# Optimization experiments

Measured on AMD Instinct MI355X. Metric: run time of the kernel, lower is better.

The kernel has to match this reference:

```python
import jax, jax.numpy as jnp
import numpy as np
from jax import lax

KSIZE = 7

def _grid():
    # torch.linspace(-7//2, 7//2, 7) == linspace(-4, 3, 7): asymmetric, step 7/6
    x = np.linspace(-4.0, 3.0, KSIZE, dtype=np.float32).reshape(-1, 1)
    y = x.T
    return x, y

def _gaussian_kernel(sigma):
    x, y = _grid()
    g = np.exp(-(x ** 2 + y ** 2) / (2.0 * sigma ** 2))
    g = g / g.sum()
    return g.reshape(1, 1, KSIZE, KSIZE).astype(np.float32)

def _log_kernel(sigma):
    x, y = _grid()
    r2 = x ** 2 + y ** 2
    log = (1.0 - r2 / (2.0 * sigma ** 2)) * np.exp(-r2 / (2.0 * sigma ** 2))
    log = log / np.abs(log).sum()
    return log.reshape(1, 1, KSIZE, KSIZE).astype(np.float32)

SOBEL_X = jnp.asarray([[-1, 0, 1], [-2, 0, 2], [-1, 0, 1]], dtype=jnp.float32).reshape(1, 1, 3, 3)
SOBEL_Y = jnp.asarray([[-1, -2, -1], [0, 0, 0], [1, 2, 1]], dtype=jnp.float32).reshape(1, 1, 3, 3)
POINT = jnp.asarray([[0, -1, 0], [-1, 4, -1], [0, -1, 0]], dtype=jnp.float32).reshape(1, 1, 3, 3)
STRUCT_FILTERS = [jnp.asarray(_gaussian_kernel(s)) for s in (0.5, 1.0, 2.0)]
SCALE_FILTERS = [jnp.asarray(_log_kernel(s)) for s in (1.0, 2.0, 4.0)]

def _conv(x, k, pad):
    # torch F.conv2d == cross-correlation, which lax conv also computes (no kernel flip)
    return lax.conv_general_dilated(
        x, k, window_strides=(1, 1),
        padding=[(pad, pad), (pad, pad)],
        dimension_numbers=("NCHW", "OIHW", "NCHW"))

def _mse(a, b):
    d = a - b
    return jnp.mean(d * d)

def _maxpool3(x):
    # torch max_pool2d pads with -inf
    return lax.reduce_window(
        x, -jnp.inf, lax.max,
        window_dimensions=(1, 1, 3, 3), window_strides=(1, 1, 1, 1),
        padding=[(0, 0), (0, 0), (1, 1), (1, 1)])

def setup_inputs() -> dict:
    key = jax.random.key(0)
    k1, k2 = jax.random.split(key)
    shape = (64, 1, 512, 512)
    return {
        "reconstruction": jax.random.normal(k1, shape, dtype=jnp.float32),
        "target": jax.random.normal(k2, shape, dtype=jnp.float32),
    }

def reference(reconstruction, target):
    # intensity-weighted reconstruction loss
    w = (target > target.mean()).astype(reconstruction.dtype) * 2.0 + 1.0
    recon_loss = _mse(reconstruction * w, target * w)

    # gradient (sobel) loss
    gradient_loss = (
        _mse(_conv(reconstruction, SOBEL_X, 1), _conv(target, SOBEL_X, 1)) +
        _mse(_conv(reconstruction, SOBEL_Y, 1), _conv(target, SOBEL_Y, 1)))

    # point-source (laplacian) loss
    point_loss = _mse(_conv(reconstruction, POINT, 1), _conv(target, POINT, 1))

    # multi-scale gaussian structure loss
    structure_loss = 0.0
    for f in STRUCT_FILTERS:
        structure_loss += _mse(_conv(reconstruction, f, KSIZE // 2), _conv(target, f, KSIZE // 2))

    # LoG blob-scale loss
    scale_loss = 0.0
    for f in SCALE_FILTERS:
        scale_loss += _mse(_conv(reconstruction, f, KSIZE // 2), _conv(target, f, KSIZE // 2))

    # peak preservation via 3x3 max pool + L1
    peak_loss = jnp.mean(jnp.abs(_maxpool3(reconstruction) - _maxpool3(target)))

    return (recon_loss + 2.0 * gradient_loss + 1.5 * point_loss +
            1.0 * structure_loss + 1.0 * scale_loss + 2.0 * peak_loss)
```

## Files before the change

### kernel.cpp

```cpp
#include <hip/hip_runtime.h>
#include <math.h>

#define IMG 512
#define IMG2 (IMG * IMG)
#define NPIX (64 * IMG2)
#define ZPB 8

__device__ float g_c[64];

typedef __fp16 h2_t __attribute__((ext_vector_type(2)));

#define OOB_SRT 0xFBFFFBFFu

__device__ __forceinline__ float rdfl(float x) {
    return __uint_as_float(__builtin_amdgcn_readfirstlane(__float_as_uint(x)));
}
__device__ __forceinline__ unsigned int rdflu(float x) {
    return __builtin_amdgcn_readfirstlane(__float_as_uint(x));
}
__device__ __forceinline__ unsigned int as_u(h2_t h) {
    union { h2_t h; unsigned int u; } c;
    c.h = h;
    return c.u;
}
__device__ __forceinline__ h2_t as_h2(unsigned int u) {
    union { unsigned int u; h2_t h; } c;
    c.u = u;
    return c.h;
}
__device__ __forceinline__ h2_t h2z() {
    h2_t z = {(__fp16)0.f, (__fp16)0.f};
    return z;
}
__device__ __forceinline__ h2_t hmax2(h2_t a, h2_t b) {
    return __builtin_elementwise_max(a, b);
}

__device__ void compute_coeffs() {
    const double step = 7.0 / 6.0;
    float x[7];
    for (int j = 0; j < 7; j++) x[j] = (float)(-4.0 + j * step);
    x[6] = 3.0f;
    const float sigs[4] = {0.5f, 1.0f, 2.0f, 4.0f};
    float E[4][7], Q[4][7], Vv[3][7];
    for (int s = 0; s < 4; s++) {
        float inv = 1.0f / (2.0f * sigs[s] * sigs[s]);
        for (int j = 0; j < 7; j++) {
            float q = x[j] * x[j] * inv;
            Q[s][j] = q;
            E[s][j] = expf(-q);
        }
    }
    for (int s = 0; s < 3; s++)
        for (int j = 0; j < 7; j++) Vv[s][j] = Q[s + 1][j] * E[s + 1][j];

    auto pk2 = [](float a, float b) -> float {
        h2_t h;
        h[0] = (__fp16)a;
        h[1] = (__fp16)b;
        union { h2_t h; float f; } c;
        c.h = h;
        return c.f;
    };
    for (int k = 0; k < 7; k++) {
        g_c[k] = pk2(E[0][k], E[1][k]);
        g_c[7 + k] = pk2(E[2][k], E[3][k]);
        g_c[14 + k] = pk2(Vv[0][k], Vv[1][k]);
        g_c[21 + k] = pk2(Vv[2][k], Vv[2][k]);
        g_c[28 + k] = pk2(E[1][k], E[2][k]);
        g_c[35 + k] = pk2(E[2][k], -Vv[2][k]);
        g_c[42 + k] = pk2(-Vv[0][k], -Vv[1][k]);
        g_c[49 + k] = pk2(E[3][k], 0.f);
    }
    for (int s = 0; s < 3; s++) {
        float gs = 0.f;
        for (int i = 0; i < 7; i++)
            for (int j = 0; j < 7; j++) gs += E[s][i] * E[s][j];
        g_c[56 + s] = 1.0f / (gs * gs);
    }
    for (int s = 1; s < 4; s++) {
        float n = 0.f;
        for (int i = 0; i < 7; i++)
            for (int j = 0; j < 7; j++) {
                float v = E[s][i] * E[s][j] * (1.0f - Q[s][i] - Q[s][j]);
                n += fabsf(v);
            }
        g_c[59 + (s - 1)] = 1.0f / (n * n);
    }
}

__global__ __launch_bounds__(256) void sum_target_kernel(const float4* __restrict__ t4,
                                                          float* __restrict__ ws) {
    if (blockIdx.x == 0 && threadIdx.x == 0) compute_coeffs();
    float s = 0.f;
    for (int i = blockIdx.x * 256 + threadIdx.x; i < NPIX / 4; i += 256 * 256) {
        float4 v = t4[i];
        s += (v.x + v.y) + (v.z + v.w);
    }
    for (int off = 32; off > 0; off >>= 1) s += __shfl_down(s, off);
    __shared__ float ps[4];
    int lane = threadIdx.x & 63, wid = threadIdx.x >> 6;
    if (lane == 0) ps[wid] = s;
    __syncthreads();
    if (threadIdx.x == 0) ws[blockIdx.x] = (ps[0] + ps[1]) + (ps[2] + ps[3]);
}

__global__ __launch_bounds__(256, 6) void main_kernel(const float* __restrict__ R,
                                                      const float* __restrict__ T,
                                                      float* __restrict__ ws) {
    __shared__ unsigned srt[38][44];
    __shared__ uint4 hrec[32][39];
    __shared__ float red[4];

    const int tid = threadIdx.x;
    const int gx0 = blockIdx.x * 32, gy0 = blockIdx.y * 32;
    const int z0 = blockIdx.z * ZPB;
    const int bid = blockIdx.x + (blockIdx.y << 4) + (blockIdx.z << 8);

    {
        float v = ws[tid];
        for (int off = 32; off > 0; off >>= 1) v += __shfl_down(v, off);
        int lane = tid & 63, wid = tid >> 6;
        if (lane == 0) red[wid] = v;
        __syncthreads();
    }
    const float mean = rdfl(((red[0] + red[1]) + (red[2] + red[3])) * (1.0f / (float)NPIX));

    h2_t cE01[7], cE23[7], cV01[7], cV2[7], d2c[7], d3c[7], d4c[7], d5c[7];
#pragma unroll
    for (int k = 0; k < 7; k++) {
        cE01[k] = as_h2(rdflu(g_c[k]));
        cE23[k] = as_h2(rdflu(g_c[7 + k]));
        cV01[k] = as_h2(rdflu(g_c[14 + k]));
        cV2[k] = as_h2(rdflu(g_c[21 + k]));
        d2c[k] = as_h2(rdflu(g_c[28 + k]));
        d3c[k] = as_h2(rdflu(g_c[35 + k]));
        d4c[k] = as_h2(rdflu(g_c[42 + k]));
        d5c[k] = as_h2(rdflu(g_c[49 + k]));
    }
    float invS4[3], invN2[3];
#pragma unroll
    for (int s = 0; s < 3; s++) {
        invS4[s] = rdfl(g_c[56 + s]);
        invN2[s] = rdfl(g_c[59 + s]);
    }

    const int q0 = tid, q1 = tid + 256;
    const bool has1 = (q1 < 380);
    const int i0 = q0 / 10, c0 = q0 - 10 * i0;
    const int i1 = q1 / 10, c1 = q1 - 10 * i1;
    const int gy_0 = gy0 + i0 - 3, gxb0 = gx0 - 4 + 4 * c0;
    const int gy_1 = gy0 + i1 - 3, gxb1 = gx0 - 4 + 4 * c1;
    const int o0 = min(max(gy_0, 0), IMG - 1) * IMG + min(max(gxb0, 0), IMG - 4);
    const int o1 = min(max(gy_1, 0), IMG - 1) * IMG + min(max(gxb1, 0), IMG - 4);
    const bool vy0 = ((unsigned)gy_0 < IMG), vy1 = ((unsigned)gy_1 < IMG);
    bool m0[4], m1[4];
#pragma unroll
    for (int e = 0; e < 4; e++) {
        m0[e] = vy0 && ((unsigned)(gxb0 + e) < IMG);
        m1[e] = vy1 && ((unsigned)(gxb1 + e) < IMG);
    }

    const int x = tid & 31;
    const int y0 = (tid >> 5) * 4;

    float4 ra, ta, rb, tb;

#define LOAD_TILE(zz)                          \
    {                                          \
        const float* Rz = R + (long)(zz)*IMG2; \
        const float* Tz = T + (long)(zz)*IMG2; \
        ra = *(const float4*)(Rz + o0);        \
        ta = *(const float4*)(Tz + o0);        \
        if (has1) {                            \
            rb = *(const float4*)(Rz + o1);    \
            tb = *(const float4*)(Tz + o1);    \
        }                                      \
    }

#define WRITE_TILE()                                                            \
    {                                                                           \
        unsigned pkq[4];                                                        \
        _Pragma("unroll") for (int e = 0; e < 4; e++) {                         \
            float rv = ((const float*)&ra)[e], tv = ((const float*)&ta)[e];     \
            pkq[e] = m0[e] ? as_u(__builtin_amdgcn_cvt_pkrtz(rv, tv)) : OOB_SRT; \
        }                                                                       \
        *(uint4*)&srt[i0][4 * c0] = make_uint4(pkq[0], pkq[1], pkq[2], pkq[3]); \
        if (has1) {                                                             \
            unsigned pkq1[4];                                                   \
            _Pragma("unroll") for (int e = 0; e < 4; e++) {                     \
                float rv = ((const float*)&rb)[e], tv = ((const float*)&tb)[e]; \
                pkq1[e] =                                                       \
                    m1[e] ? as_u(__builtin_amdgcn_cvt_pkrtz(rv, tv)) : OOB_SRT; \
            }                                                                   \
            *(uint4*)&srt[i1][4 * c1] =                                         \
                make_uint4(pkq1[0], pkq1[1], pkq1[2], pkq1[3]);                 \
        }                                                                       \
    }

    LOAD_TILE(z0);
    WRITE_TILE();
    __syncthreads();

    float total = 0.f;

    for (int it = 0; it < ZPB; ++it) {
        const bool havenext = (it + 1 < ZPB);
        if (havenext) LOAD_TILE(z0 + it + 1);

        {
            h2_t w_[6][3];
#pragma unroll
            for (int r = 0; r < 6; r++)
#pragma unroll
                for (int c = 0; c < 3; c++) w_[r][c] = as_h2(srt[y0 + 2 + r][x + 3 + c]);
            __fp16 dcol[6][3];
            h2_t cm[6];
            float tc[6];
#pragma unroll
            for (int r = 0; r < 6; r++) {
#pragma unroll
                for (int c = 0; c < 3; c++) dcol[r][c] = w_[r][c][0] - w_[r][c][1];
                cm[r] = hmax2(hmax2(w_[r][0], w_[r][1]), w_[r][2]);
                tc[r] = (float)w_[r][1][1];
            }
            __fp16 rx[6], rs[6];
#pragma unroll
            for (int r = 0; r < 6; r++) {
                rx[r] = dcol[r][2] - dcol[r][0];
                rs[r] = dcol[r][0] + (__fp16)2.f * dcol[r][1] + dcol[r][2];
            }
#pragma unroll
            for (int yy = 0; yy < 4; yy++) {
                float sx = (float)(rx[yy] + (__fp16)2.f * rx[yy + 1] + rx[yy + 2]);
                float sy = (float)(rs[yy + 2] - rs[yy]);
                float pt = (float)((__fp16)4.f * dcol[yy + 1][1] - dcol[yy][1] -
                                   dcol[yy + 2][1] - dcol[yy + 1][0] - dcol[yy + 1][2]);
                float d = (float)dcol[yy + 1][1];
                float w2 = (tc[yy + 1] > mean) ? 9.f : 1.f;
                h2_t wm = hmax2(hmax2(cm[yy], cm[yy + 1]), cm[yy + 2]);
                float mr = (float)wm[0], mt = (float)wm[1];
                total += w2 * d * d + 2.f * (sx * sx + sy * sy) + 1.5f * pt * pt +
                         2.f * fabsf(mr - mt);
            }
        }

        for (int j = tid; j < 304; j += 256) {
            int xq = j / 38, y = j - 38 * xq;
            const unsigned* rp = &srt[y][4 * xq];
            uint4 A = *(const uint4*)(rp);
            uint4 B = *(const uint4*)(rp + 4);
            uint4 C = *(const uint4*)(rp + 8);
            unsigned uw[12] = {A.x, A.y, A.z, A.w, B.x, B.y, B.z, B.w, C.x, C.y, C.z, C.w};
            h2_t wp[10];
#pragma unroll
            for (int i = 0; i < 10; i++) {
                h2_t v = as_h2(uw[i + 1]);
                __fp16 d = v[0] - v[1];
                h2_t dd;
                dd[0] = d;
                dd[1] = d;
                wp[i] = dd;
            }
#pragma unroll
            for (int p = 0; p < 4; p++) {
                h2_t aE01 = h2z(), aE23 = h2z(), aV01 = h2z(), aV2 = h2z();
#pragma unroll
                for (int k = 0; k < 7; k++) {
                    h2_t d = wp[p + k];
                    aE01 = cE01[k] * d + aE01;
                    aE23 = cE23[k] * d + aE23;
                    aV01 = cV01[k] * d + aV01;
                    aV2 = cV2[k] * d + aV2;
                }
                h2_t he12 = __builtin_shufflevector(aE01, aE23, 1, 2);
                h2_t tm01 = he12 - aV01;
                h2_t he33 = __builtin_shufflevector(aE23, aE23, 1, 1);
                h2_t tm22 = he33 - aV2;
                hrec[4 * xq + p][y] =
                    make_uint4(as_u(aE01), as_u(aE23), as_u(tm01), as_u(tm22));
            }
        }
        __syncthreads();

        if (havenext) WRITE_TILE();

        {
            h2_t A1[4], A2[4], A3[4], A4[4], A5[4];
#pragma unroll
            for (int yy = 0; yy < 4; yy++) {
                A1[yy] = h2z();
                A2[yy] = h2z();
                A3[yy] = h2z();
                A4[yy] = h2z();
                A5[yy] = h2z();
            }
#pragma unroll
            for (int q = 0; q < 10; q++) {
                uint4 rec = hrec[x][y0 + q];
                h2_t rx = as_h2(rec.x), ry = as_h2(rec.y);
                h2_t rz = as_h2(rec.z), rw = as_h2(rec.w);
                h2_t r12 = __builtin_shufflevector(rx, ry, 1, 2);
#pragma unroll
                for (int yy = 0; yy < 4; yy++) {
                    const int k = q - yy;
                    if (k >= 0 && k <= 6) {
                        A1[yy] = cE01[k] * rx + A1[yy];
                        A2[yy] = d2c[k] * rz + A2[yy];
                        A3[yy] = d3c[k] * ry + A3[yy];
                        A4[yy] = d4c[k] * r12 + A4[yy];
                        A5[yy] = d5c[k] * rw + A5[yy];
                    }
                }
            }
#pragma unroll
            for (int yy = 0; yy < 4; yy++) {
                h2_t Bp = A2[yy] + A4[yy];
                float g0 = (float)A1[yy][0], g1 = (float)A1[yy][1];
                float g2 = (float)A3[yy][0];
                float aL0 = (float)Bp[0], aL1 = (float)Bp[1];
                float aL2 = (float)A5[yy][0] + (float)A3[yy][1];
                total += invS4[0] * g0 * g0 + invS4[1] * g1 * g1 + invS4[2] * g2 * g2 +
                         invN2[0] * aL0 * aL0 + invN2[1] * aL1 * aL1 + invN2[2] * aL2 * aL2;
            }
        }
        __syncthreads();
    }

    for (int off = 32; off > 0; off >>= 1) total += __shfl_down(total, off);
    int lane = tid & 63, wid = tid >> 6;
    if (lane == 0) red[wid] = total;
    __syncthreads();
    if (tid == 0) ws[256 + bid] = (red[0] + red[1]) + (red[2] + red[3]);
}

__global__ __launch_bounds__(256) void finalize_kernel(const float* __restrict__ ws,
                                                       float* __restrict__ out) {
    float s = 0.f;
    for (int i = threadIdx.x; i < 2048; i += 256) s += ws[256 + i];
    for (int off = 32; off > 0; off >>= 1) s += __shfl_down(s, off);
    __shared__ float ps[4];
    int lane = threadIdx.x & 63, wid = threadIdx.x >> 6;
    if (lane == 0) ps[wid] = s;
    __syncthreads();
    if (threadIdx.x == 0)
        out[0] = ((ps[0] + ps[1]) + (ps[2] + ps[3])) * (1.0f / (float)NPIX);
}

extern "C" void kernel_launch(void* const* d_in, const int* in_sizes, int n_in,
                              void* d_out, int out_size, void* d_ws, size_t ws_size,
                              hipStream_t stream) {
    const float* recon = (const float*)d_in[0];
    const float* target = (const float*)d_in[1];
    float* ws = (float*)d_ws;

    hipLaunchKernelGGL(sum_target_kernel, dim3(256), dim3(256), 0, stream,
                       (const float4*)target, ws);
    dim3 grid(16, 16, 64 / ZPB), block(256);
    hipLaunchKernelGGL(main_kernel, grid, block, 0, stream, recon, target, ws);
    hipLaunchKernelGGL(finalize_kernel, dim3(1), dim3(256), 0, stream, ws, (float*)d_out);
}
```

Baseline: 110.2 us.

## Double tile height to 64 rows, halve z per block, 8 rows per thread

```diff
diff --git a/kernel.cpp b/kernel.cpp
--- a/kernel.cpp
+++ b/kernel.cpp
@@ -4,7 +4,8 @@
 #define IMG 512
 #define IMG2 (IMG * IMG)
 #define NPIX (64 * IMG2)
-#define ZPB 8
+#define ZPB 4
+#define NQ 700
 
 __device__ float g_c[64];
 
@@ -105,17 +106,17 @@
     if (threadIdx.x == 0) ws[blockIdx.x] = (ps[0] + ps[1]) + (ps[2] + ps[3]);
 }
 
-__global__ __launch_bounds__(256, 6) void main_kernel(const float* __restrict__ R,
+__global__ __launch_bounds__(256, 3) void main_kernel(const float* __restrict__ R,
                                                       const float* __restrict__ T,
                                                       float* __restrict__ ws) {
-    __shared__ unsigned srt[38][44];
-    __shared__ uint4 hrec[32][39];
+    __shared__ unsigned srt[70][44];
+    __shared__ uint4 hrec[32][71];
     __shared__ float red[4];
 
     const int tid = threadIdx.x;
-    const int gx0 = blockIdx.x * 32, gy0 = blockIdx.y * 32;
+    const int gx0 = blockIdx.x * 32, gy0 = blockIdx.y * 64;
     const int z0 = blockIdx.z * ZPB;
-    const int bid = blockIdx.x + (blockIdx.y << 4) + (blockIdx.z << 8);
+    const int bid = blockIdx.x + (blockIdx.y << 4) + (blockIdx.z << 7);
 
     {
         float v = ws[tid];
@@ -145,57 +146,50 @@
         invN2[s] = rdfl(g_c[59 + s]);
     }
 
-    const int q0 = tid, q1 = tid + 256;
-    const bool has1 = (q1 < 380);
-    const int i0 = q0 / 10, c0 = q0 - 10 * i0;
-    const int i1 = q1 / 10, c1 = q1 - 10 * i1;
-    const int gy_0 = gy0 + i0 - 3, gxb0 = gx0 - 4 + 4 * c0;
-    const int gy_1 = gy0 + i1 - 3, gxb1 = gx0 - 4 + 4 * c1;
-    const int o0 = min(max(gy_0, 0), IMG - 1) * IMG + min(max(gxb0, 0), IMG - 4);
-    const int o1 = min(max(gy_1, 0), IMG - 1) * IMG + min(max(gxb1, 0), IMG - 4);
-    const bool vy0 = ((unsigned)gy_0 < IMG), vy1 = ((unsigned)gy_1 < IMG);
-    bool m0[4], m1[4];
-#pragma unroll
-    for (int e = 0; e < 4; e++) {
-        m0[e] = vy0 && ((unsigned)(gxb0 + e) < IMG);
-        m1[e] = vy1 && ((unsigned)(gxb1 + e) < IMG);
+    int iq[3], cq[3], oo[3];
+    bool hq[3], mm[3][4];
+#pragma unroll
+    for (int e = 0; e < 3; e++) {
+        int q = tid + e * 256;
+        hq[e] = (q < NQ);
+        int qs = hq[e] ? q : (NQ - 1);
+        int i = qs / 10, c = qs - 10 * i;
+        iq[e] = i;
+        cq[e] = c;
+        int gy = gy0 + i - 3, gxb = gx0 - 4 + 4 * c;
+        oo[e] = min(max(gy, 0), IMG - 1) * IMG + min(max(gxb, 0), IMG - 4);
+        bool vy = ((unsigned)gy < IMG);
+#pragma unroll
+        for (int k = 0; k < 4; k++) mm[e][k] = vy && ((unsigned)(gxb + k) < IMG);
     }
 
     const int x = tid & 31;
-    const int y0 = (tid >> 5) * 4;
-
-    float4 ra, ta, rb, tb;
-
-#define LOAD_TILE(zz)                          \
-    {                                          \
-        const float* Rz = R + (long)(zz)*IMG2; \
-        const float* Tz = T + (long)(zz)*IMG2; \
-        ra = *(const float4*)(Rz + o0);        \
-        ta = *(const float4*)(Tz + o0);        \
-        if (has1) {                            \
-            rb = *(const float4*)(Rz + o1);    \
-            tb = *(const float4*)(Tz + o1);    \
-        }                                      \
-    }
-
-#define WRITE_TILE()                                                            \
-    {                                                                           \
-        unsigned pkq[4];                                                        \
-        _Pragma("unroll") for (int e = 0; e < 4; e++) {                         \
-            float rv = ((const float*)&ra)[e], tv = ((const float*)&ta)[e];     \
-            pkq[e] = m0[e] ? as_u(__builtin_amdgcn_cvt_pkrtz(rv, tv)) : OOB_SRT; \
-        }                                                                       \
-        *(uint4*)&srt[i0][4 * c0] = make_uint4(pkq[0], pkq[1], pkq[2], pkq[3]); \
-        if (has1) {                                                             \
-            unsigned pkq1[4];                                                   \
-            _Pragma("unroll") for (int e = 0; e < 4; e++) {                     \
-                float rv = ((const float*)&rb)[e], tv = ((const float*)&tb)[e]; \
-                pkq1[e] =                                                       \
-                    m1[e] ? as_u(__builtin_amdgcn_cvt_pkrtz(rv, tv)) : OOB_SRT; \
-            }                                                                   \
-            *(uint4*)&srt[i1][4 * c1] =                                         \
-                make_uint4(pkq1[0], pkq1[1], pkq1[2], pkq1[3]);                 \
-        }                                                                       \
+    const int Y0 = (tid >> 5) * 8;
+
+    float4 rr[3], tt[3];
+
+#define LOAD_TILE(zz)                               \
+    {                                               \
+        const float* Rz = R + (long)(zz)*IMG2;      \
+        const float* Tz = T + (long)(zz)*IMG2;      \
+        _Pragma("unroll") for (int e = 0; e < 3; e++) if (hq[e]) { \
+            rr[e] = *(const float4*)(Rz + oo[e]);   \
+            tt[e] = *(const float4*)(Tz + oo[e]);   \
+        }                                           \
+    }
+
+#define WRITE_TILE()                                                              \
+    {                                                                             \
+        _Pragma("unroll") for (int e = 0; e < 3; e++) if (hq[e]) {                \
+            unsigned pk[4];                                                       \
+            _Pragma("unroll") for (int k2 = 0; k2 < 4; k2++) {                    \
+                float rv = ((const float*)&rr[e])[k2];                            \
+                float tv = ((const float*)&tt[e])[k2];                            \
+                pk[k2] = mm[e][k2] ? as_u(__builtin_amdgcn_cvt_pkrtz(rv, tv))     \
+                                   : OOB_SRT;                                     \
+            }                                                                     \
+            *(uint4*)&srt[iq[e]][4 * cq[e]] = make_uint4(pk[0], pk[1], pk[2], pk[3]); \
+        }                                                                         \
     }
 
     LOAD_TILE(z0);
@@ -208,12 +202,14 @@
         const bool havenext = (it + 1 < ZPB);
         if (havenext) LOAD_TILE(z0 + it + 1);
 
-        {
+#pragma unroll
+        for (int g = 0; g < 2; g++) {
+            const int yb = Y0 + 4 * g;
             h2_t w_[6][3];
 #pragma unroll
             for (int r = 0; r < 6; r++)
 #pragma unroll
-                for (int c = 0; c < 3; c++) w_[r][c] = as_h2(srt[y0 + 2 + r][x + 3 + c]);
+                for (int c = 0; c < 3; c++) w_[r][c] = as_h2(srt[yb + 2 + r][x + 3 + c]);
             __fp16 dcol[6][3];
             h2_t cm[6];
             float tc[6];
@@ -245,8 +241,8 @@
             }
         }
 
-        for (int j = tid; j < 304; j += 256) {
-            int xq = j / 38, y = j - 38 * xq;
+        for (int j = tid; j < 560; j += 256) {
+            int xq = j / 70, y = j - 70 * xq;
             const unsigned* rp = &srt[y][4 * xq];
             uint4 A = *(const uint4*)(rp);
             uint4 B = *(const uint4*)(rp + 4);
@@ -286,9 +282,9 @@
         if (havenext) WRITE_TILE();
 
         {
-            h2_t A1[4], A2[4], A3[4], A4[4], A5[4];
-#pragma unroll
-            for (int yy = 0; yy < 4; yy++) {
+            h2_t A1[8], A2[8], A3[8], A4[8], A5[8];
+#pragma unroll
+            for (int yy = 0; yy < 8; yy++) {
                 A1[yy] = h2z();
                 A2[yy] = h2z();
                 A3[yy] = h2z();
@@ -296,13 +292,13 @@
                 A5[yy] = h2z();
             }
 #pragma unroll
-            for (int q = 0; q < 10; q++) {
-                uint4 rec = hrec[x][y0 + q];
+            for (int q = 0; q < 14; q++) {
+                uint4 rec = hrec[x][Y0 + q];
                 h2_t rx = as_h2(rec.x), ry = as_h2(rec.y);
                 h2_t rz = as_h2(rec.z), rw = as_h2(rec.w);
                 h2_t r12 = __builtin_shufflevector(rx, ry, 1, 2);
 #pragma unroll
-                for (int yy = 0; yy < 4; yy++) {
+                for (int yy = 0; yy < 8; yy++) {
                     const int k = q - yy;
                     if (k >= 0 && k <= 6) {
                         A1[yy] = cE01[k] * rx + A1[yy];
@@ -314,7 +310,7 @@
                 }
             }
 #pragma unroll
-            for (int yy = 0; yy < 4; yy++) {
+            for (int yy = 0; yy < 8; yy++) {
                 h2_t Bp = A2[yy] + A4[yy];
                 float g0 = (float)A1[yy][0], g1 = (float)A1[yy][1];
                 float g2 = (float)A3[yy][0];
@@ -356,7 +352,7 @@
 
     hipLaunchKernelGGL(sum_target_kernel, dim3(256), dim3(256), 0, stream,
                        (const float4*)target, ws);
-    dim3 grid(16, 16, 64 / ZPB), block(256);
+    dim3 grid(16, 8, 64 / ZPB), block(256);
     hipLaunchKernelGGL(main_kernel, grid, block, 0, stream, recon, target, ws);
     hipLaunchKernelGGL(finalize_kernel, dim3(1), dim3(256), 0, stream, ws, (float*)d_out);
 }
```

Result: slower. 114.1 us (+3.6%).
